# Optimization experiments

Hardware: AMD Instinct MI355X
Metric: run time of the kernel (lower is better)

Reference implementation:

```python
import jax, jax.numpy as jnp
import numpy as np
from functools import partial

N_QUBITS = 8
DEPTH = 2
DIM = 2 ** N_QUBITS


@jax.checkpoint
def quantum_expval(angles):
    """Batched statevector sim of the PennyLane circuit.

    angles: [B, n_qubits] real. Circuit (repeated DEPTH times, same angles
    each layer, matching params.repeat(1, depth, 1)):
      RX(angles[w]) on every wire, then CNOT(w, w+1) chain.
    Returns <Z_0> per sample, shape [B].
    """
    B = angles.shape[0]
    c = jnp.cos(angles * 0.5).astype(jnp.complex64)
    s = jnp.sin(angles * 0.5).astype(jnp.complex64)
    state = jnp.zeros((B, DIM), jnp.complex64).at[:, 0].set(1.0)
    for _ in range(DEPTH):
        for w in range(N_QUBITS):
            # wire 0 is the most-significant bit (PennyLane convention)
            st = state.reshape(B, 2 ** w, 2, DIM // 2 ** (w + 1))
            cw = c[:, w][:, None, None]
            sw = s[:, w][:, None, None]
            a0, a1 = st[:, :, 0], st[:, :, 1]
            state = jnp.stack([cw * a0 - 1j * sw * a1,
                               -1j * sw * a0 + cw * a1], axis=2).reshape(B, DIM)
        for w in range(N_QUBITS - 1):
            # CNOT(control=w, target=w+1): flip target amplitudes when control=1
            st = state.reshape(B, 2 ** w, 2, 2, DIM // 2 ** (w + 2))
            flipped = st[:, :, 1, ::-1, :]
            state = jnp.concatenate([st[:, :, 0:1], flipped[:, :, None]], axis=2).reshape(B, DIM)
    p = jnp.real(state * jnp.conj(state)).reshape(B, 2, DIM // 2)
    return (p[:, 0].sum(-1) - p[:, 1].sum(-1)).astype(angles.dtype)


def qgate(combined, Wl, bl, Wq, bq):
    h = combined @ Wl.T + bl          # [B, hidden]
    ang = h @ Wq.T + bq               # [B, n_qubits]
    return quantum_expval(ang)        # [B]


def setup_inputs() -> dict:
    T, B, I, H, Q = 256, 256, 256, 256, N_QUBITS
    key = jax.random.key(0)
    ks = jax.random.split(key, 17)
    sc_l = 1.0 / np.sqrt(I + H)
    sc_q = 1.0 / np.sqrt(H)
    d = {"inputs": jax.random.normal(ks[0], (T, B, I), jnp.float32)}
    names = ["f", "i", "u", "o"]
    for j, n in enumerate(names):
        d[f"W{n}"] = jax.random.normal(ks[1 + j], (H, I + H), jnp.float32) * sc_l
        d[f"b{n}"] = jnp.zeros((H,), jnp.float32)
        d[f"W{n}q"] = jax.random.normal(ks[5 + j], (Q, H), jnp.float32) * sc_q
        d[f"b{n}q"] = jnp.zeros((Q,), jnp.float32)
    return d


def reference(inputs, Wf, bf, Wfq, bfq, Wi, bi, Wiq, biq,
              Wu, bu, Wuq, buq, Wo, bo, Woq, boq):
    T, B, _ = inputs.shape
    H = Wf.shape[0]
    h0 = jnp.zeros((B, H), inputs.dtype)
    c0 = jnp.zeros((B, H), inputs.dtype)

    def step(carry, x):
        hx, cx = carry
        comb = jnp.concatenate([x, hx], axis=1)          # [B, I+H]
        f = jax.nn.sigmoid(qgate(comb, Wf, bf, Wfq, bfq))[:, None]
        i = jax.nn.sigmoid(qgate(comb, Wi, bi, Wiq, biq))[:, None]
        g = jnp.tanh(qgate(comb, Wu, bu, Wuq, buq))[:, None]
        o = jax.nn.sigmoid(qgate(comb, Wo, bo, Woq, boq))[:, None]
        cx = f * cx + i * g
        hx = o * jnp.tanh(cx)
        return (hx, cx), hx

    (hx, cx), outputs = jax.lax.scan(step, (h0, c0), inputs)
    return outputs, (hx, cx)
```

## Files before the change

### kernel.cpp

```cpp
#include <hip/hip_runtime.h>

#define T_DIM 256
#define B_DIM 256
#define I_DIM 256
#define H_DIM 256
#define COMB  512
#define JCH   16
#define DEPTH 8
#define CHUNK 8
#define WARM  16
#define NCH   (T_DIM / CHUNK)
#define REPS  32
#define DGRID 2048
#define DIT   8

typedef float f32x4 __attribute__((ext_vector_type(4)));

#define OFF_W    0
#define OFF_PS   1024
#define OFF_BETA 1056
#define OFF_A    1152

__global__ __launch_bounds__(512) void k_w1(
    const float* W0, const float* Q0, const float* B0, const float* q0,
    const float* W1, const float* Q1, const float* B1, const float* q1,
    const float* W2, const float* Q2, const float* B2, const float* q2,
    const float* W3, const float* Q3, const float* B3, const float* q3,
    float* __restrict__ ws) {
  const float* W[4] = {W0, W1, W2, W3};
  const float* Q[4] = {Q0, Q1, Q2, Q3};
  const float* Bv[4] = {B0, B1, B2, B3};
  const float* qv[4] = {q0, q1, q2, q3};
  const int g = blockIdx.x >> 4, jc = blockIdx.x & (JCH - 1);
  const int tid = threadIdx.x;
  const int jj = tid & 31;
  const int ks = tid >> 5;
  const int j0 = jc * 32;
  const float* Wg = W[g];
  const float* Qg = Q[g];

  float acc = 0.f;
#pragma unroll
  for (int kk = 0; kk < 16; ++kk) {
    const int k = ks * 16 + kk;
    acc = fmaf(Qg[k], Wg[(size_t)k * COMB + j0 + jj], acc);
  }

  __shared__ float red[512];
  red[tid] = acc;
  __syncthreads();
  for (int s = 256; s >= 32; s >>= 1) {
    if (tid < s) red[tid] += red[tid + s];
    __syncthreads();
  }

  if (jc < 8) {
    if (tid < 32) ws[OFF_W + g * I_DIM + j0 + tid] = red[tid];
  } else {
    if (tid < 16) red[tid] += red[tid + 16];
    __syncthreads();
    if (tid < 8) red[tid] += red[tid + 8];
    __syncthreads();
    if (tid < 4) red[tid] += red[tid + 4];
    __syncthreads();
    if (tid < 2) red[tid] += red[tid + 2];
    __syncthreads();
    if (tid == 0) ws[OFF_PS + g * 8 + (jc - 8)] = red[0] + red[1];
  }

  if (jc == 0) {
    __syncthreads();
    red[tid] = (tid < H_DIM) ? Qg[tid] * Bv[g][tid] : 0.f;
    __syncthreads();
    for (int s = 256; s > 0; s >>= 1) {
      if (tid < s) red[tid] += red[tid + s];
      __syncthreads();
    }
    if (tid == 0) ws[OFF_BETA + g] = red[0] + qv[g][0];
  }
}

__global__ __launch_bounds__(256) void k_dots(const float* __restrict__ x,
                                              float* __restrict__ ws) {
  __shared__ float wx[4 * I_DIM];
  const int tid = threadIdx.x;
  const int bid = blockIdx.x;

#pragma unroll
  for (int e = 0; e < 4; ++e) wx[tid + e * 256] = ws[OFF_W + tid + e * 256];
  __syncthreads();

  const float bb0 = ws[OFF_BETA + 0], bb1 = ws[OFF_BETA + 1];
  const float bb2 = ws[OFF_BETA + 2], bb3 = ws[OFF_BETA + 3];
  const int wave = tid >> 6, lane = tid & 63;
  const float4* wx4 = reinterpret_cast<const float4*>(wx);
  const float4 w0 = wx4[0 * 64 + lane];
  const float4 w1 = wx4[1 * 64 + lane];
  const float4 w2 = wx4[2 * 64 + lane];
  const float4 w3 = wx4[3 * 64 + lane];
  float4* A4o = reinterpret_cast<float4*>(ws + OFF_A);
#pragma unroll
  for (int it = 0; it < DIT; ++it) {
    const int row = it * (DGRID * 4) + bid * 4 + wave;
    const f32x4 xv = __builtin_nontemporal_load(
        reinterpret_cast<const f32x4*>(x + (size_t)row * I_DIM) + lane);
    float p0 = xv.x * w0.x + xv.y * w0.y + xv.z * w0.z + xv.w * w0.w;
    float p1 = xv.x * w1.x + xv.y * w1.y + xv.z * w1.z + xv.w * w1.w;
    float p2 = xv.x * w2.x + xv.y * w2.y + xv.z * w2.z + xv.w * w2.w;
    float p3 = xv.x * w3.x + xv.y * w3.y + xv.z * w3.z + xv.w * w3.w;
#pragma unroll
    for (int off = 32; off > 0; off >>= 1) {
      p0 += __shfl_down(p0, off, 64);
      p1 += __shfl_down(p1, off, 64);
      p2 += __shfl_down(p2, off, 64);
      p3 += __shfl_down(p3, off, 64);
    }
    if (lane == 0) {
      float4 r = {2.f * (p0 + bb0), 2.f * (p1 + bb1), 2.f * (p2 + bb2),
                  2.f * (p3 + bb3)};
      A4o[row] = r;
    }
  }
}

#define C0S 0.6224593312f
#define C1S 0.1175018561f
#define C2S (-0.0071946125f)
#define C3S (-0.0020074354f)
#define C4S 0.0002728000f

#define G0T 0.4621171573f
#define G1T 0.3932238600f
#define G2T (-0.0908577800f)
#define G3T (-0.0117749000f)
#define G4T 0.0102923100f
#define G5T (-0.0008507100f)

__device__ __forceinline__ float poly_sig(float u) {
  return fmaf(u, fmaf(u, fmaf(u, fmaf(u, C4S, C3S), C2S), C1S), C0S);
}
__device__ __forceinline__ float poly_tanhE(float u) {
  return fmaf(u, fmaf(u, fmaf(u, fmaf(u, fmaf(u, G5T, G4T), G3T), G2T), G1T), G0T);
}
__device__ __forceinline__ float pade_tanh(float x) {
  const float y = x * x;
  const float num = fmaf(y, fmaf(y, 1.0f, 105.0f), 945.0f);
  const float den = fmaf(y, fmaf(y, 15.0f, 420.0f), 945.0f);
  return x * num * __builtin_amdgcn_rcpf(den);
}

__global__ __launch_bounds__(256) void k_scanb(const float* __restrict__ ws,
                                               float* __restrict__ out) {
  const int bid = blockIdx.x, tid = threadIdx.x;
  const int c = (NCH - 1) - (bid >> 5);
  const int rep = bid & (REPS - 1);
  const int b = tid;
  const int t0 = c * CHUNK;
  const int w0 = (t0 - WARM > 0) ? (t0 - WARM) : 0;
  const int NS = t0 + CHUNK - w0;

  __shared__ float lds_h[CHUNK][B_DIM];
  __shared__ float lds_hc[2][B_DIM];

  float sg[4];
#pragma unroll
  for (int g = 0; g < 4; ++g) {
    float a = 0.f;
#pragma unroll
    for (int p = 0; p < 8; ++p) a += ws[OFF_PS + g * 8 + p];
    sg[g] = 2.f * a;
  }
  const float s0 = sg[0], s1 = sg[1], s2 = sg[2], s3 = sg[3];

  float C = 0.f, Hs = 0.f;
  const float4* A4 = reinterpret_cast<const float4*>(ws + OFF_A);

  float4 buf[DEPTH];
#pragma unroll
  for (int j = 0; j < DEPTH; ++j) buf[j] = A4[(w0 + j) * B_DIM + b];

#define STEP(a, tt)                                        \
  {                                                        \
    const float uf = __cosf(fmaf(Hs, s0, (a).x));          \
    const float ui = __cosf(fmaf(Hs, s1, (a).y));          \
    const float uu = __cosf(fmaf(Hs, s2, (a).z));          \
    const float uo = __cosf(fmaf(Hs, s3, (a).w));          \
    const float f = poly_sig(uf);                          \
    const float i = poly_sig(ui);                          \
    const float g = poly_tanhE(uu);                        \
    const float o = poly_sig(uo);                          \
    C = fmaf(f, C, i * g);                                 \
    Hs = o * pade_tanh(C);                                 \
    if ((tt) >= t0) lds_h[(tt)-t0][b] = Hs;                \
  }

  for (int sb = 0; sb < NS; sb += DEPTH) {
#pragma unroll
    for (int j = 0; j < DEPTH; ++j) {
      const float4 a = buf[j];
      if (sb + DEPTH + j < NS)
        buf[j] = A4[(w0 + sb + DEPTH + j) * B_DIM + b];
      STEP(a, w0 + sb + j);
    }
  }
#undef STEP

  lds_hc[0][b] = Hs;
  lds_hc[1][b] = C;
  __syncthreads();

  f32x4* o4 = reinterpret_cast<f32x4*>(out);
#pragma unroll
  for (int it = 0; it < 16; ++it) {
    const int idx = it * 256 + tid;
    const int ts = idx >> 9;
    const int rem = idx & 511;
    const int bb = rem >> 6;
    const int f4 = rem & 63;
    const float v = lds_h[ts][rep * 8 + bb];
    const f32x4 r = {v, v, v, v};
    __builtin_nontemporal_store(
        r, o4 + ((size_t)((t0 + ts) * B_DIM + rep * 8 + bb)) * 64 + f4);
  }
  if (c == NCH - 1) {
    const size_t N1 = (size_t)T_DIM * B_DIM * (H_DIM / 4);
#pragma unroll
    for (int it = 0; it < 2; ++it) {
      const int idx = it * 256 + tid;
      const int bb = idx >> 6;
      const int f4 = idx & 63;
      const float vh = lds_hc[0][rep * 8 + bb];
      const float vc = lds_hc[1][rep * 8 + bb];
      const f32x4 rh = {vh, vh, vh, vh};
      const f32x4 rc = {vc, vc, vc, vc};
      __builtin_nontemporal_store(rh,
                                  o4 + N1 + ((size_t)(rep * 8 + bb)) * 64 + f4);
      __builtin_nontemporal_store(
          rc, o4 + N1 + B_DIM * 64 + ((size_t)(rep * 8 + bb)) * 64 + f4);
    }
  }
}

extern "C" void kernel_launch(void* const* d_in, const int* in_sizes, int n_in,
                              void* d_out, int out_size, void* d_ws,
                              size_t ws_size, hipStream_t stream) {
  const float* x = (const float*)d_in[0];
  const float* Wf = (const float*)d_in[1];
  const float* bf = (const float*)d_in[2];
  const float* Wfq = (const float*)d_in[3];
  const float* bfq = (const float*)d_in[4];
  const float* Wi = (const float*)d_in[5];
  const float* bi = (const float*)d_in[6];
  const float* Wiq = (const float*)d_in[7];
  const float* biq = (const float*)d_in[8];
  const float* Wu = (const float*)d_in[9];
  const float* bu = (const float*)d_in[10];
  const float* Wuq = (const float*)d_in[11];
  const float* buq = (const float*)d_in[12];
  const float* Wo = (const float*)d_in[13];
  const float* bo = (const float*)d_in[14];
  const float* Woq = (const float*)d_in[15];
  const float* boq = (const float*)d_in[16];

  float* ws = (float*)d_ws;
  float* out = (float*)d_out;

  k_w1<<<4 * JCH, 512, 0, stream>>>(Wf, Wfq, bf, bfq, Wi, Wiq, bi, biq, Wu,
                                    Wuq, bu, buq, Wo, Woq, bo, boq, ws);
  k_dots<<<DGRID, 256, 0, stream>>>(x, ws);
  k_scanb<<<NCH * REPS, 256, 0, stream>>>(ws, out);
}
```

Before: 45.98 us.

## Fuse input projection into scan kernel, computing per-block rows into LDS

Removes the separate k_dots kernel. Each scan block now projects only the x rows it needs (its warmup window plus its chunk, for its 8 batch columns) and writes them to LDS instead of a global workspace. The scan itself now runs on just 8 threads per block for their own batches, instead of every block redundantly scanning all 256 batches. The trade-off is that x rows in the warmup overlap are read and projected by several blocks, which multiplies input traffic unless the cache absorbs it, and each wave's projection loop is serial and latency-bound.

Measured after the change: 76.49 us. 1.66x slower.

```diff
diff --git a/kernel.cpp b/kernel.cpp
--- a/kernel.cpp
+++ b/kernel.cpp
@@ -6,20 +6,17 @@
 #define H_DIM 256
 #define COMB  512
 #define JCH   16
-#define DEPTH 8
 #define CHUNK 8
 #define WARM  16
+#define NSMAX (WARM + CHUNK)
 #define NCH   (T_DIM / CHUNK)
 #define REPS  32
-#define DGRID 2048
-#define DIT   8
 
 typedef float f32x4 __attribute__((ext_vector_type(4)));
 
 #define OFF_W    0
 #define OFF_PS   1024
 #define OFF_BETA 1056
-#define OFF_A    1152
 
 __global__ __launch_bounds__(512) void k_w1(
     const float* W0, const float* Q0, const float* B0, const float* q0,
@@ -80,49 +77,6 @@
   }
 }
 
-__global__ __launch_bounds__(256) void k_dots(const float* __restrict__ x,
-                                              float* __restrict__ ws) {
-  __shared__ float wx[4 * I_DIM];
-  const int tid = threadIdx.x;
-  const int bid = blockIdx.x;
-
-#pragma unroll
-  for (int e = 0; e < 4; ++e) wx[tid + e * 256] = ws[OFF_W + tid + e * 256];
-  __syncthreads();
-
-  const float bb0 = ws[OFF_BETA + 0], bb1 = ws[OFF_BETA + 1];
-  const float bb2 = ws[OFF_BETA + 2], bb3 = ws[OFF_BETA + 3];
-  const int wave = tid >> 6, lane = tid & 63;
-  const float4* wx4 = reinterpret_cast<const float4*>(wx);
-  const float4 w0 = wx4[0 * 64 + lane];
-  const float4 w1 = wx4[1 * 64 + lane];
-  const float4 w2 = wx4[2 * 64 + lane];
-  const float4 w3 = wx4[3 * 64 + lane];
-  float4* A4o = reinterpret_cast<float4*>(ws + OFF_A);
-#pragma unroll
-  for (int it = 0; it < DIT; ++it) {
-    const int row = it * (DGRID * 4) + bid * 4 + wave;
-    const f32x4 xv = __builtin_nontemporal_load(
-        reinterpret_cast<const f32x4*>(x + (size_t)row * I_DIM) + lane);
-    float p0 = xv.x * w0.x + xv.y * w0.y + xv.z * w0.z + xv.w * w0.w;
-    float p1 = xv.x * w1.x + xv.y * w1.y + xv.z * w1.z + xv.w * w1.w;
-    float p2 = xv.x * w2.x + xv.y * w2.y + xv.z * w2.z + xv.w * w2.w;
-    float p3 = xv.x * w3.x + xv.y * w3.y + xv.z * w3.z + xv.w * w3.w;
-#pragma unroll
-    for (int off = 32; off > 0; off >>= 1) {
-      p0 += __shfl_down(p0, off, 64);
-      p1 += __shfl_down(p1, off, 64);
-      p2 += __shfl_down(p2, off, 64);
-      p3 += __shfl_down(p3, off, 64);
-    }
-    if (lane == 0) {
-      float4 r = {2.f * (p0 + bb0), 2.f * (p1 + bb1), 2.f * (p2 + bb2),
-                  2.f * (p3 + bb3)};
-      A4o[row] = r;
-    }
-  }
-}
-
 #define C0S 0.6224593312f
 #define C1S 0.1175018561f
 #define C2S (-0.0071946125f)
@@ -149,64 +103,91 @@
   return x * num * __builtin_amdgcn_rcpf(den);
 }
 
-__global__ __launch_bounds__(256) void k_scanb(const float* __restrict__ ws,
+__global__ __launch_bounds__(256) void k_fused(const float* __restrict__ x,
+                                               const float* __restrict__ ws,
                                                float* __restrict__ out) {
   const int bid = blockIdx.x, tid = threadIdx.x;
-  const int c = (NCH - 1) - (bid >> 5);
+  const int c = bid >> 5;
   const int rep = bid & (REPS - 1);
-  const int b = tid;
   const int t0 = c * CHUNK;
-  const int w0 = (t0 - WARM > 0) ? (t0 - WARM) : 0;
+  const int w0 = (t0 > WARM) ? (t0 - WARM) : 0;
   const int NS = t0 + CHUNK - w0;
 
-  __shared__ float lds_h[CHUNK][B_DIM];
-  __shared__ float lds_hc[2][B_DIM];
-
-  float sg[4];
-#pragma unroll
-  for (int g = 0; g < 4; ++g) {
-    float a = 0.f;
-#pragma unroll
-    for (int p = 0; p < 8; ++p) a += ws[OFF_PS + g * 8 + p];
-    sg[g] = 2.f * a;
-  }
-  const float s0 = sg[0], s1 = sg[1], s2 = sg[2], s3 = sg[3];
-
-  float C = 0.f, Hs = 0.f;
-  const float4* A4 = reinterpret_cast<const float4*>(ws + OFF_A);
-
-  float4 buf[DEPTH];
-#pragma unroll
-  for (int j = 0; j < DEPTH; ++j) buf[j] = A4[(w0 + j) * B_DIM + b];
-
-#define STEP(a, tt)                                        \
-  {                                                        \
-    const float uf = __cosf(fmaf(Hs, s0, (a).x));          \
-    const float ui = __cosf(fmaf(Hs, s1, (a).y));          \
-    const float uu = __cosf(fmaf(Hs, s2, (a).z));          \
-    const float uo = __cosf(fmaf(Hs, s3, (a).w));          \
-    const float f = poly_sig(uf);                          \
-    const float i = poly_sig(ui);                          \
-    const float g = poly_tanhE(uu);                        \
-    const float o = poly_sig(uo);                          \
-    C = fmaf(f, C, i * g);                                 \
-    Hs = o * pade_tanh(C);                                 \
-    if ((tt) >= t0) lds_h[(tt)-t0][b] = Hs;                \
-  }
-
-  for (int sb = 0; sb < NS; sb += DEPTH) {
-#pragma unroll
-    for (int j = 0; j < DEPTH; ++j) {
-      const float4 a = buf[j];
-      if (sb + DEPTH + j < NS)
-        buf[j] = A4[(w0 + sb + DEPTH + j) * B_DIM + b];
-      STEP(a, w0 + sb + j);
-    }
-  }
-#undef STEP
-
-  lds_hc[0][b] = Hs;
-  lds_hc[1][b] = C;
+  __shared__ float wx[4 * I_DIM];
+  __shared__ f32x4 a_lds[NSMAX][8];
+  __shared__ float lds_h[CHUNK][8];
+  __shared__ float lds_hc[2][8];
+
+#pragma unroll
+  for (int e = 0; e < 4; ++e) wx[tid + e * 256] = ws[OFF_W + tid + e * 256];
+  __syncthreads();
+
+  {
+    const int wave = tid >> 6, lane = tid & 63;
+    const float bb0 = ws[OFF_BETA + 0], bb1 = ws[OFF_BETA + 1];
+    const float bb2 = ws[OFF_BETA + 2], bb3 = ws[OFF_BETA + 3];
+    const float4* wx4 = reinterpret_cast<const float4*>(wx);
+    const float4 w0v = wx4[0 * 64 + lane];
+    const float4 w1v = wx4[1 * 64 + lane];
+    const float4 w2v = wx4[2 * 64 + lane];
+    const float4 w3v = wx4[3 * 64 + lane];
+    const int nrows = NS * 8;
+    for (int ri = wave; ri < nrows; ri += 4) {
+      const int ts = ri >> 3, bb = ri & 7;
+      const int row = (w0 + ts) * B_DIM + rep * 8 + bb;
+      const float4 xv =
+          reinterpret_cast<const float4*>(x + (size_t)row * I_DIM)[lane];
+      float p0 = xv.x * w0v.x + xv.y * w0v.y + xv.z * w0v.z + xv.w * w0v.w;
+      float p1 = xv.x * w1v.x + xv.y * w1v.y + xv.z * w1v.z + xv.w * w1v.w;
+      float p2 = xv.x * w2v.x + xv.y * w2v.y + xv.z * w2v.z + xv.w * w2v.w;
+      float p3 = xv.x * w3v.x + xv.y * w3v.y + xv.z * w3v.z + xv.w * w3v.w;
+#pragma unroll
+      for (int off = 32; off > 0; off >>= 1) {
+        p0 += __shfl_down(p0, off, 64);
+        p1 += __shfl_down(p1, off, 64);
+        p2 += __shfl_down(p2, off, 64);
+        p3 += __shfl_down(p3, off, 64);
+      }
+      if (lane == 0) {
+        const f32x4 rr = {2.f * (p0 + bb0), 2.f * (p1 + bb1), 2.f * (p2 + bb2),
+                          2.f * (p3 + bb3)};
+        a_lds[ts][bb] = rr;
+      }
+    }
+  }
+  __syncthreads();
+
+  if (tid < 8) {
+    float sg[4];
+#pragma unroll
+    for (int g = 0; g < 4; ++g) {
+      float a = 0.f;
+#pragma unroll
+      for (int p = 0; p < 8; ++p) a += ws[OFF_PS + g * 8 + p];
+      sg[g] = 2.f * a;
+    }
+    const float s0 = sg[0], s1 = sg[1], s2 = sg[2], s3 = sg[3];
+    float C = 0.f, Hs = 0.f;
+    const int kofs = NS - CHUNK;
+    f32x4 nxt = a_lds[0][tid];
+    for (int ts = 0; ts < NS; ++ts) {
+      const f32x4 a = nxt;
+      if (ts + 1 < NS) nxt = a_lds[ts + 1][tid];
+      const float uf = __cosf(fmaf(Hs, s0, a.x));
+      const float ui = __cosf(fmaf(Hs, s1, a.y));
+      const float uu = __cosf(fmaf(Hs, s2, a.z));
+      const float uo = __cosf(fmaf(Hs, s3, a.w));
+      const float f = poly_sig(uf);
+      const float i = poly_sig(ui);
+      const float g = poly_tanhE(uu);
+      const float o = poly_sig(uo);
+      C = fmaf(f, C, i * g);
+      Hs = o * pade_tanh(C);
+      if (ts >= kofs) lds_h[ts - kofs][tid] = Hs;
+    }
+    lds_hc[0][tid] = Hs;
+    lds_hc[1][tid] = C;
+  }
   __syncthreads();
 
   f32x4* o4 = reinterpret_cast<f32x4*>(out);
@@ -217,7 +198,7 @@
     const int rem = idx & 511;
     const int bb = rem >> 6;
     const int f4 = rem & 63;
-    const float v = lds_h[ts][rep * 8 + bb];
+    const float v = lds_h[ts][bb];
     const f32x4 r = {v, v, v, v};
     __builtin_nontemporal_store(
         r, o4 + ((size_t)((t0 + ts) * B_DIM + rep * 8 + bb)) * 64 + f4);
@@ -229,12 +210,12 @@
       const int idx = it * 256 + tid;
       const int bb = idx >> 6;
       const int f4 = idx & 63;
-      const float vh = lds_hc[0][rep * 8 + bb];
-      const float vc = lds_hc[1][rep * 8 + bb];
+      const float vh = lds_hc[0][bb];
+      const float vc = lds_hc[1][bb];
       const f32x4 rh = {vh, vh, vh, vh};
       const f32x4 rc = {vc, vc, vc, vc};
-      __builtin_nontemporal_store(rh,
-                                  o4 + N1 + ((size_t)(rep * 8 + bb)) * 64 + f4);
+      __builtin_nontemporal_store(
+          rh, o4 + N1 + ((size_t)(rep * 8 + bb)) * 64 + f4);
       __builtin_nontemporal_store(
           rc, o4 + N1 + B_DIM * 64 + ((size_t)(rep * 8 + bb)) * 64 + f4);
     }
@@ -267,6 +248,5 @@
 
   k_w1<<<4 * JCH, 512, 0, stream>>>(Wf, Wfq, bf, bfq, Wi, Wiq, bi, biq, Wu,
                                     Wuq, bu, buq, Wo, Woq, bo, boq, ws);
-  k_dots<<<DGRID, 256, 0, stream>>>(x, ws);
-  k_scanb<<<NCH * REPS, 256, 0, stream>>>(ws, out);
-}
+  k_fused<<<NCH * REPS, 256, 0, stream>>>(x, ws, out);
+}
```
